# Kernel optimization log

Hardware: AMD Instinct MI355X
Metric: run time of the kernel (lower is better)

Reference implementation:

```python
import jax, jax.numpy as jnp
import numpy as np

B, S, D, H = 2, 2048, 1024, 16
HD = D // H  # head dim = 64


def setup_inputs() -> dict:
    key = jax.random.key(0)
    k1, k2, k3, k4 = jax.random.split(key, 4)
    x = jax.random.normal(k1, (B, S, D), dtype=jnp.float32)
    context = jax.random.normal(k2, (B, S, D), dtype=jnp.float32)
    Wq = jax.random.normal(k3, (D, D), dtype=jnp.float32) * 0.02   # to_query weight [out,in]
    Wkv = jax.random.normal(k4, (2 * D, D), dtype=jnp.float32) * 0.02  # to_key_value weight [out,in]
    return {"x": x, "context": context, "Wq": Wq, "Wkv": Wkv}


def reference(x, context, Wq, Wkv):
    b, i, _ = x.shape
    j = context.shape[1]
    # projections (torch Linear: y = x @ W.T)
    q = x @ Wq.T                      # [b, i, D]
    kv = context @ Wkv.T              # [b, j, 2D]
    k, v = kv[..., :D], kv[..., D:]
    # split heads: (h c) ordering -> reshape last dim to [H, HD]
    q = q.reshape(b, i, H, HD).transpose(0, 2, 1, 3)  # [b,h,i,c]
    k = k.reshape(b, j, H, HD).transpose(0, 2, 1, 3)  # [b,h,j,c]
    v = v.reshape(b, j, H, HD).transpose(0, 2, 1, 3)  # [b,h,j,c]
    q = q * (HD ** -0.5)
    scores = jnp.einsum('bhic,bhjc->bhij', q, k)      # [b,h,i,j]
    scores = scores - jax.lax.stop_gradient(scores.max(axis=-1, keepdims=True))
    attn = jax.nn.softmax(scores, axis=-1)
    out = jnp.einsum('bhij,bhjc->bhic', attn, v)      # [b,h,i,c]
    out = out.transpose(0, 2, 1, 3).reshape(b, i, H * HD)  # 'b h n d -> b n (h d)'
    return out
```

## Files before the change

### kernel.cpp

```cpp
#include <hip/hip_runtime.h>
#include <hip/hip_bf16.h>
#include <stdint.h>

typedef unsigned short u16;
typedef __attribute__((ext_vector_type(8))) __bf16 bf16x8;
typedef __attribute__((ext_vector_type(4))) float f32x4;
typedef __attribute__((ext_vector_type(16))) float f32x16;

#define AS1(p) ((const __attribute__((address_space(1))) void*)(p))
#define AS3(p) ((__attribute__((address_space(3))) void*)(p))

__device__ __forceinline__ u16 f2bf(float f) {
  union { float f; uint32_t u; } c; c.f = f;
  uint32_t u = c.u;
  u += 0x7fffu + ((u >> 16) & 1u);
  return (u16)(u >> 16);
}

__device__ __forceinline__ float exp2_fast(float x) {
  float r; asm("v_exp_f32 %0, %1" : "=v"(r) : "v"(x)); return r;
}

__global__ __launch_bounds__(256) void cast4_f32_bf16(
    const float4* __restrict__ s0, ushort4* __restrict__ d0, int n0,
    const float4* __restrict__ s1, ushort4* __restrict__ d1, int n1,
    const float4* __restrict__ s2, ushort4* __restrict__ d2, int n2,
    const float4* __restrict__ s3, ushort4* __restrict__ d3, int n3) {
  int bid = blockIdx.x;
  const float4* src; ushort4* dst; int n4, b0, nb;
  if (bid < 512)       { src = s0; dst = d0; n4 = n0; b0 = 0;    nb = 512; }
  else if (bid < 1024) { src = s1; dst = d1; n4 = n1; b0 = 512;  nb = 512; }
  else if (bid < 1152) { src = s2; dst = d2; n4 = n2; b0 = 1024; nb = 128; }
  else                 { src = s3; dst = d3; n4 = n3; b0 = 1152; nb = 256; }
  int stride = nb * 256;
  for (int i = (bid - b0) * 256 + threadIdx.x; i < n4; i += stride) {
    float4 v = src[i];
    ushort4 o;
    o.x = f2bf(v.x); o.y = f2bf(v.y); o.z = f2bf(v.z); o.w = f2bf(v.w);
    dst[i] = o;
  }
}

__global__ __launch_bounds__(256) void gemm_fused(const u16* __restrict__ xb,
                                                  const u16* __restrict__ wqb,
                                                  u16* __restrict__ qo,
                                                  const u16* __restrict__ cb,
                                                  const u16* __restrict__ wkb,
                                                  u16* __restrict__ kvo,
                                                  float scale_q) {
  __shared__ u16 As[2][128 * 32];
  __shared__ u16 Bs[2][128 * 32];
  const int K = 1024;
  int bid = blockIdx.x;
  const u16 *A, *B; u16* C; int N, bm, bn; float scale;
  if (bid < 256) { A = xb; B = wqb; C = qo;  N = 1024; bm = bid >> 3; bn = bid & 7;  scale = scale_q; }
  else { int b2 = bid - 256; A = cb; B = wkb; C = kvo; N = 2048; bm = b2 >> 4; bn = b2 & 15; scale = 1.0f; }

  int tid = threadIdx.x;
  int w = tid >> 6, l = tid & 63;
  int wr = w >> 1, wc = w & 1;
  int lr = l & 15, lg = l >> 4;

  const u16* Abase = A + (size_t)(bm * 128 + (l >> 2)) * K + (l & 3) * 8;
  const u16* Bbase = B + (size_t)(bn * 128 + (l >> 2)) * K + (l & 3) * 8;

  f32x4 acc[4][4];
#pragma unroll
  for (int i = 0; i < 4; ++i)
#pragma unroll
    for (int j = 0; j < 4; ++j) acc[i][j] = (f32x4){0.f, 0.f, 0.f, 0.f};

#define STAGE(buf, k0)                                                              \
  {                                                                                 \
    _Pragma("unroll")                                                               \
    for (int t2 = 0; t2 < 2; ++t2) {                                                \
      int seg = w * 2 + t2;                                                         \
      __builtin_amdgcn_global_load_lds(AS1(Abase + (size_t)seg * 16 * K + (k0)),    \
                                       AS3(&As[buf][seg * 512]), 16, 0, 0);         \
      __builtin_amdgcn_global_load_lds(AS1(Bbase + (size_t)seg * 16 * K + (k0)),    \
                                       AS3(&Bs[buf][seg * 512]), 16, 0, 0);         \
    }                                                                               \
  }

  STAGE(0, 0);
  for (int t = 0; t < 32; ++t) {
    int cur = t & 1;
    if (t < 31) {
      STAGE(cur ^ 1, (t + 1) * 32);
      asm volatile("s_waitcnt vmcnt(4)" ::: "memory");
    } else {
      asm volatile("s_waitcnt vmcnt(0)" ::: "memory");
    }
    __builtin_amdgcn_s_barrier();
    bf16x8 af[4], bb[4];
#pragma unroll
    for (int i = 0; i < 4; ++i)
      af[i] = *(const bf16x8*)(&As[cur][(wr * 64 + i * 16 + lr) * 32 + lg * 8]);
#pragma unroll
    for (int j = 0; j < 4; ++j)
      bb[j] = *(const bf16x8*)(&Bs[cur][(wc * 64 + j * 16 + lr) * 32 + lg * 8]);
    asm volatile("s_waitcnt lgkmcnt(0)" ::: "memory");
    __builtin_amdgcn_sched_barrier(0);
#pragma unroll
    for (int i = 0; i < 4; ++i)
#pragma unroll
      for (int j = 0; j < 4; ++j)
        acc[i][j] = __builtin_amdgcn_mfma_f32_16x16x32_bf16(af[i], bb[j], acc[i][j], 0, 0, 0);
    __builtin_amdgcn_s_barrier();
  }
#undef STAGE

#pragma unroll
  for (int i = 0; i < 4; ++i)
#pragma unroll
    for (int j = 0; j < 4; ++j)
#pragma unroll
      for (int r = 0; r < 4; ++r) {
        int row = bm * 128 + wr * 64 + i * 16 + lg * 4 + r;
        int col = bn * 128 + wc * 64 + j * 16 + lr;
        C[(size_t)row * N + col] = f2bf(acc[i][j][r] * scale);
      }
}

#define SQ 2048

__global__ __launch_bounds__(256, 2) void attn_kernel(const u16* __restrict__ Q,
                                                      const u16* __restrict__ KV,
                                                      float* __restrict__ O) {
  __shared__ u16 Ks[2 * 64 * 64];
  __shared__ u16 Vt[2 * 64 * 64];

  int qt = blockIdx.x & 15;
  int bh = blockIdx.x >> 4;
  int b = bh >> 4, h = bh & 15;
  int tid = threadIdx.x;
  int w = tid >> 6, l = tid & 63;
  int li = l & 31, hi = l >> 5;
  int jr = l >> 3, bk = l & 7;

  const u16* kbase = KV + (size_t)b * SQ * 2048 + (size_t)h * 64;
  const u16* vbase = kbase + 1024;
  int i0g = qt * 128 + w * 32;
  const u16* qrow = Q + (size_t)(b * SQ + i0g + li) * 1024 + h * 64;

  bf16x8 qf0 = *(const bf16x8*)(qrow + 0  + hi * 8);
  bf16x8 qf1 = *(const bf16x8*)(qrow + 16 + hi * 8);
  bf16x8 qf2 = *(const bf16x8*)(qrow + 32 + hi * 8);
  bf16x8 qf3 = *(const bf16x8*)(qrow + 48 + hi * 8);

  {
    const u16* gk0 = kbase + (size_t)(w * 8 + jr) * 2048 + ((bk ^ jr) * 8);
    __builtin_amdgcn_global_load_lds(AS1(gk0), AS3(Ks + w * 512), 16, 0, 0);
    const u16* gk1 = kbase + (size_t)(32 + w * 8 + jr) * 2048 + ((bk ^ jr) * 8);
    __builtin_amdgcn_global_load_lds(AS1(gk1), AS3(Ks + 2048 + w * 512), 16, 0, 0);
  }
  uint4 vregA = *(const uint4*)(vbase + (size_t)(tid >> 3) * 2048 + (tid & 7) * 8);
  uint4 vregB = *(const uint4*)(vbase + (size_t)(32 + (tid >> 3)) * 2048 + (tid & 7) * 8);

  float m_run = -1e30f, l_run = 0.f;
  f32x16 acc0, acc1;
#pragma unroll
  for (int r = 0; r < 16; ++r) { acc0[r] = 0.f; acc1[r] = 0.f; }

  for (int t = 0; t < SQ / 64; ++t) {
    int cur = t & 1;
    u16* Ksc = Ks + cur * 4096;
    u16* Vtc = Vt + cur * 4096;
    __syncthreads();
    {
      int a = tid & 7, jj0 = tid >> 3;
      const u16* pa_ = (const u16*)&vregA;
#pragma unroll
      for (int e = 0; e < 8; ++e)
        *(u16*)((char*)Vtc + (a * 8 + e) * 128 + ((jj0 * 2) ^ ((e ^ a) << 4))) = pa_[e];
      const u16* pb_ = (const u16*)&vregB;
      int jj1 = 32 + jj0;
#pragma unroll
      for (int e = 0; e < 8; ++e)
        *(u16*)((char*)Vtc + (a * 8 + e) * 128 + ((jj1 * 2) ^ ((e ^ a) << 4))) = pb_[e];
    }
    __syncthreads();
    if (t + 1 < SQ / 64) {
      int nxt = cur ^ 1;
      int j0n = (t + 1) * 64;
      const u16* gk0 = kbase + (size_t)(j0n + w * 8 + jr) * 2048 + ((bk ^ jr) * 8);
      __builtin_amdgcn_global_load_lds(AS1(gk0), AS3(Ks + nxt * 4096 + w * 512), 16, 0, 0);
      const u16* gk1 = kbase + (size_t)(j0n + 32 + w * 8 + jr) * 2048 + ((bk ^ jr) * 8);
      __builtin_amdgcn_global_load_lds(AS1(gk1), AS3(Ks + nxt * 4096 + 2048 + w * 512), 16, 0, 0);
      vregA = *(const uint4*)(vbase + (size_t)(j0n + (tid >> 3)) * 2048 + (tid & 7) * 8);
      vregB = *(const uint4*)(vbase + (size_t)(j0n + 32 + (tid >> 3)) * 2048 + (tid & 7) * 8);
    }
    f32x16 s0, s1;
#pragma unroll
    for (int r = 0; r < 16; ++r) { s0[r] = 0.f; s1[r] = 0.f; }
    int swk = (li & 7) << 4;
    __builtin_amdgcn_s_setprio(1);
#pragma unroll
    for (int kb = 0; kb < 4; ++kb) {
      bf16x8 k0 = *(const bf16x8*)((const char*)Ksc + li * 128        + ((kb * 32 + hi * 16) ^ swk));
      bf16x8 k1 = *(const bf16x8*)((const char*)Ksc + (32 + li) * 128 + ((kb * 32 + hi * 16) ^ swk));
      bf16x8 qq = (kb == 0) ? qf0 : (kb == 1) ? qf1 : (kb == 2) ? qf2 : qf3;
      s0 = __builtin_amdgcn_mfma_f32_32x32x16_bf16(k0, qq, s0, 0, 0, 0);
      s1 = __builtin_amdgcn_mfma_f32_32x32x16_bf16(k1, qq, s1, 0, 0, 0);
    }
    __builtin_amdgcn_s_setprio(0);
    float pm = fmaxf(s0[0], s0[1]);
#pragma unroll
    for (int r = 2; r < 16; r += 2) pm = fmaxf(fmaxf(pm, s0[r]), s0[r + 1]);
#pragma unroll
    for (int r = 0; r < 16; r += 2) pm = fmaxf(fmaxf(pm, s1[r]), s1[r + 1]);
    pm = fmaxf(pm, __shfl_xor(pm, 32));
    if (!__all(pm <= m_run + 8.0f)) {
      float mnew = fmaxf(m_run, pm);
      float esc = exp2_fast(m_run - mnew);
      m_run = mnew;
      l_run *= esc;
#pragma unroll
      for (int r = 0; r < 16; ++r) { acc0[r] *= esc; acc1[r] *= esc; }
    }
    float p0[16], p1[16];
    float sum = 0.f;
#pragma unroll
    for (int r = 0; r < 16; ++r) { p0[r] = exp2_fast(s0[r] - m_run); sum += p0[r]; }
#pragma unroll
    for (int r = 0; r < 16; ++r) { p1[r] = exp2_fast(s1[r] - m_run); sum += p1[r]; }
    sum += __shfl_xor(sum, 32);
    l_run += sum;
    unsigned pw[16];
#pragma unroll
    for (int i2 = 0; i2 < 8; ++i2) {
      asm("v_cvt_pk_bf16_f32 %0, %1, %2" : "=v"(pw[i2])     : "v"(p0[2 * i2]), "v"(p0[2 * i2 + 1]));
      asm("v_cvt_pk_bf16_f32 %0, %1, %2" : "=v"(pw[8 + i2]) : "v"(p1[2 * i2]), "v"(p1[2 * i2 + 1]));
    }
#pragma unroll
    for (int gB = 0; gB < 2; ++gB) {
      int o = gB * 8;
      asm volatile("v_permlane32_swap_b32 %0, %1" : "+v"(pw[o + 0]), "+v"(pw[o + 2]));
      asm volatile("v_permlane32_swap_b32 %0, %1" : "+v"(pw[o + 1]), "+v"(pw[o + 3]));
      asm volatile("v_permlane32_swap_b32 %0, %1" : "+v"(pw[o + 4]), "+v"(pw[o + 6]));
      asm volatile("v_permlane32_swap_b32 %0, %1" : "+v"(pw[o + 5]), "+v"(pw[o + 7]));
    }
    __builtin_amdgcn_s_setprio(1);
#pragma unroll
    for (int kb2 = 0; kb2 < 4; ++kb2) {
      uint4 ufr;
      ufr.x = pw[kb2 * 4 + 0]; ufr.y = pw[kb2 * 4 + 1];
      ufr.z = pw[kb2 * 4 + 2]; ufr.w = pw[kb2 * 4 + 3];
      bf16x8 pa = *(bf16x8*)&ufr;
      int jbyte = kb2 * 32 + hi * 16;
      int d0_ = li, d1_ = 32 + li;
      bf16x8 v0 = *(const bf16x8*)((const char*)Vtc + d0_ * 128 + (jbyte ^ (((d0_ ^ (d0_ >> 3)) & 7) << 4)));
      bf16x8 v1 = *(const bf16x8*)((const char*)Vtc + d1_ * 128 + (jbyte ^ (((d1_ ^ (d1_ >> 3)) & 7) << 4)));
      acc0 = __builtin_amdgcn_mfma_f32_32x32x16_bf16(v0, pa, acc0, 0, 0, 0);
      acc1 = __builtin_amdgcn_mfma_f32_32x32x16_bf16(v1, pa, acc1, 0, 0, 0);
    }
    __builtin_amdgcn_s_setprio(0);
  }
  float inv = 1.f / l_run;
  float* orow = O + ((size_t)(b * SQ + i0g + li) * 1024 + h * 64);
#pragma unroll
  for (int g = 0; g < 4; ++g) {
    f32x4 o0, o1;
#pragma unroll
    for (int q_ = 0; q_ < 4; ++q_) {
      o0[q_] = acc0[g * 4 + q_] * inv;
      o1[q_] = acc1[g * 4 + q_] * inv;
    }
    *(f32x4*)(orow + 8 * g + 4 * hi) = o0;
    *(f32x4*)(orow + 32 + 8 * g + 4 * hi) = o1;
  }
}

extern "C" void kernel_launch(void* const* d_in, const int* in_sizes, int n_in,
                              void* d_out, int out_size, void* d_ws, size_t ws_size,
                              hipStream_t stream) {
  (void)in_sizes; (void)n_in; (void)out_size; (void)ws_size;
  const float* x   = (const float*)d_in[0];
  const float* ctx = (const float*)d_in[1];
  const float* Wq  = (const float*)d_in[2];
  const float* Wkv = (const float*)d_in[3];
  float* out = (float*)d_out;
  char* ws = (char*)d_ws;

  u16* xb  = (u16*)(ws);
  u16* cb  = (u16*)(ws + (8ull  << 20));
  u16* wqb = (u16*)(ws + (16ull << 20));
  u16* wkb = (u16*)(ws + (18ull << 20));
  u16* q   = (u16*)(ws + (22ull << 20));
  u16* kv  = (u16*)(ws + (30ull << 20));

  cast4_f32_bf16<<<1408, 256, 0, stream>>>(
      (const float4*)x,   (ushort4*)xb,  (4096 * 1024) / 4,
      (const float4*)ctx, (ushort4*)cb,  (4096 * 1024) / 4,
      (const float4*)Wq,  (ushort4*)wqb, (1024 * 1024) / 4,
      (const float4*)Wkv, (ushort4*)wkb, (2048 * 1024) / 4);

  gemm_fused<<<768, 256, 0, stream>>>(xb, wqb, q, cb, wkb, kv, 0.125f * 1.44269504f);

  attn_kernel<<<512, 256, 0, stream>>>(q, kv, out);
}
```

Before: 114.1 us.

## Triple-buffer GEMM, remap blocks across XCDs, widen attention KV tile to 128

The projection GEMM moves from double to triple-buffered LDS staging with a two-tile prefetch depth, and remaps block IDs so consecutive blocks spread across the 8 XCDs. The attention kernel doubles its K/V tile from 64 to 128 keys per iteration, which halves the loop trips, barriers and softmax rescale checks. It also gives the attention kernel the same XCD-aware block remapping and restructures the QK^T MFMA chains. In exchange LDS use and register pressure rise (four score accumulators, 32 packed words), which could lower occupancy under the 2-blocks-per-CU bound.

Result: faster. 99.01 us (-13.3%).

```diff
diff --git a/kernel.cpp b/kernel.cpp
--- a/kernel.cpp
+++ b/kernel.cpp
@@ -48,10 +48,10 @@
                                                   const u16* __restrict__ wkb,
                                                   u16* __restrict__ kvo,
                                                   float scale_q) {
-  __shared__ u16 As[2][128 * 32];
-  __shared__ u16 Bs[2][128 * 32];
+  __shared__ u16 As[3][128 * 32];
+  __shared__ u16 Bs[3][128 * 32];
   const int K = 1024;
-  int bid = blockIdx.x;
+  int bid = (blockIdx.x & 7) * 96 + (blockIdx.x >> 3);
   const u16 *A, *B; u16* C; int N, bm, bn; float scale;
   if (bid < 256) { A = xb; B = wqb; C = qo;  N = 1024; bm = bid >> 3; bn = bid & 7;  scale = scale_q; }
   else { int b2 = bid - 256; A = cb; B = wkb; C = kvo; N = 2048; bm = b2 >> 4; bn = b2 & 15; scale = 1.0f; }
@@ -83,10 +83,14 @@
   }
 
   STAGE(0, 0);
+  STAGE(1, 32);
+  int cur = 0;
   for (int t = 0; t < 32; ++t) {
-    int cur = t & 1;
-    if (t < 31) {
-      STAGE(cur ^ 1, (t + 1) * 32);
+    if (t < 30) {
+      int pf = cur + 2; if (pf >= 3) pf -= 3;
+      STAGE(pf, (t + 2) * 32);
+      asm volatile("s_waitcnt vmcnt(8)" ::: "memory");
+    } else if (t == 30) {
       asm volatile("s_waitcnt vmcnt(4)" ::: "memory");
     } else {
       asm volatile("s_waitcnt vmcnt(0)" ::: "memory");
@@ -107,6 +111,7 @@
       for (int j = 0; j < 4; ++j)
         acc[i][j] = __builtin_amdgcn_mfma_f32_16x16x32_bf16(af[i], bb[j], acc[i][j], 0, 0, 0);
     __builtin_amdgcn_s_barrier();
+    if (++cur == 3) cur = 0;
   }
 #undef STAGE
 
@@ -123,20 +128,23 @@
 }
 
 #define SQ 2048
+#define NTT 16
 
 __global__ __launch_bounds__(256, 2) void attn_kernel(const u16* __restrict__ Q,
                                                       const u16* __restrict__ KV,
                                                       float* __restrict__ O) {
-  __shared__ u16 Ks[2 * 64 * 64];
-  __shared__ u16 Vt[2 * 64 * 64];
-
-  int qt = blockIdx.x & 15;
-  int bh = blockIdx.x >> 4;
+  __shared__ u16 Ks[2][128 * 64];
+  __shared__ u16 Vt[2][64 * 128];
+
+  int wgid = (blockIdx.x & 7) * 64 + (blockIdx.x >> 3);
+  int qt = wgid & 15;
+  int bh = wgid >> 4;
   int b = bh >> 4, h = bh & 15;
   int tid = threadIdx.x;
   int w = tid >> 6, l = tid & 63;
   int li = l & 31, hi = l >> 5;
   int jr = l >> 3, bk = l & 7;
+  int a7 = tid & 7, jj = tid >> 3;
 
   const u16* kbase = KV + (size_t)b * SQ * 2048 + (size_t)h * 64;
   const u16* vbase = kbase + 1024;
@@ -148,67 +156,88 @@
   bf16x8 qf2 = *(const bf16x8*)(qrow + 32 + hi * 8);
   bf16x8 qf3 = *(const bf16x8*)(qrow + 48 + hi * 8);
 
-  {
-    const u16* gk0 = kbase + (size_t)(w * 8 + jr) * 2048 + ((bk ^ jr) * 8);
-    __builtin_amdgcn_global_load_lds(AS1(gk0), AS3(Ks + w * 512), 16, 0, 0);
-    const u16* gk1 = kbase + (size_t)(32 + w * 8 + jr) * 2048 + ((bk ^ jr) * 8);
-    __builtin_amdgcn_global_load_lds(AS1(gk1), AS3(Ks + 2048 + w * 512), 16, 0, 0);
-  }
-  uint4 vregA = *(const uint4*)(vbase + (size_t)(tid >> 3) * 2048 + (tid & 7) * 8);
-  uint4 vregB = *(const uint4*)(vbase + (size_t)(32 + (tid >> 3)) * 2048 + (tid & 7) * 8);
+#pragma unroll
+  for (int c = 0; c < 4; ++c) {
+    const u16* gk = kbase + (size_t)(c * 32 + w * 8 + jr) * 2048 + ((bk ^ jr) * 8);
+    __builtin_amdgcn_global_load_lds(AS1(gk), AS3(&Ks[0][c * 2048 + w * 512]), 16, 0, 0);
+  }
+  uint4 vrA = *(const uint4*)(vbase + (size_t)(jj +  0) * 2048 + a7 * 8);
+  uint4 vrB = *(const uint4*)(vbase + (size_t)(jj + 32) * 2048 + a7 * 8);
+  uint4 vrC = *(const uint4*)(vbase + (size_t)(jj + 64) * 2048 + a7 * 8);
+  uint4 vrD = *(const uint4*)(vbase + (size_t)(jj + 96) * 2048 + a7 * 8);
 
   float m_run = -1e30f, l_run = 0.f;
-  f32x16 acc0, acc1;
-#pragma unroll
-  for (int r = 0; r < 16; ++r) { acc0[r] = 0.f; acc1[r] = 0.f; }
-
-  for (int t = 0; t < SQ / 64; ++t) {
-    int cur = t & 1;
-    u16* Ksc = Ks + cur * 4096;
-    u16* Vtc = Vt + cur * 4096;
+  f32x16 acc0, acc1, zz;
+#pragma unroll
+  for (int r = 0; r < 16; ++r) { acc0[r] = 0.f; acc1[r] = 0.f; zz[r] = 0.f; }
+
+  int swk = (li & 7) << 4;
+  int sw0 = ((li ^ (li >> 3)) & 7) << 4;
+  int sw1 = (((32 + li) ^ ((32 + li) >> 3)) & 7) << 4;
+
+  for (int t = 0; t < NTT; ++t) {
+    u16* Ksc = (u16*)Ks[t & 1];
+    char* Vtc = (char*)Vt[t & 1];
     __syncthreads();
     {
-      int a = tid & 7, jj0 = tid >> 3;
-      const u16* pa_ = (const u16*)&vregA;
-#pragma unroll
-      for (int e = 0; e < 8; ++e)
-        *(u16*)((char*)Vtc + (a * 8 + e) * 128 + ((jj0 * 2) ^ ((e ^ a) << 4))) = pa_[e];
-      const u16* pb_ = (const u16*)&vregB;
-      int jj1 = 32 + jj0;
-#pragma unroll
-      for (int e = 0; e < 8; ++e)
-        *(u16*)((char*)Vtc + (a * 8 + e) * 128 + ((jj1 * 2) ^ ((e ^ a) << 4))) = pb_[e];
-    }
-    __syncthreads();
-    if (t + 1 < SQ / 64) {
-      int nxt = cur ^ 1;
-      int j0n = (t + 1) * 64;
-      const u16* gk0 = kbase + (size_t)(j0n + w * 8 + jr) * 2048 + ((bk ^ jr) * 8);
-      __builtin_amdgcn_global_load_lds(AS1(gk0), AS3(Ks + nxt * 4096 + w * 512), 16, 0, 0);
-      const u16* gk1 = kbase + (size_t)(j0n + 32 + w * 8 + jr) * 2048 + ((bk ^ jr) * 8);
-      __builtin_amdgcn_global_load_lds(AS1(gk1), AS3(Ks + nxt * 4096 + 2048 + w * 512), 16, 0, 0);
-      vregA = *(const uint4*)(vbase + (size_t)(j0n + (tid >> 3)) * 2048 + (tid & 7) * 8);
-      vregB = *(const uint4*)(vbase + (size_t)(j0n + 32 + (tid >> 3)) * 2048 + (tid & 7) * 8);
-    }
-    f32x16 s0, s1;
-#pragma unroll
-    for (int r = 0; r < 16; ++r) { s0[r] = 0.f; s1[r] = 0.f; }
-    int swk = (li & 7) << 4;
+      const u16* pA = (const u16*)&vrA;
+      const u16* pB = (const u16*)&vrB;
+      const u16* pC = (const u16*)&vrC;
+      const u16* pD = (const u16*)&vrD;
+#pragma unroll
+      for (int e = 0; e < 8; ++e) {
+        int dbyte = (a7 * 8 + e) * 256, sw = (e ^ a7) << 4;
+        *(u16*)(Vtc + dbyte + (((jj * 2) +   0) ^ sw)) = pA[e];
+        *(u16*)(Vtc + dbyte + (((jj * 2) +  64) ^ sw)) = pB[e];
+        *(u16*)(Vtc + dbyte + (((jj * 2) + 128) ^ sw)) = pC[e];
+        *(u16*)(Vtc + dbyte + (((jj * 2) + 192) ^ sw)) = pD[e];
+      }
+    }
+    asm volatile("s_waitcnt lgkmcnt(0)" ::: "memory");
+    __builtin_amdgcn_s_barrier();
+    if (t + 1 < NTT) {
+      int j0n = (t + 1) * 128;
+      u16* Ksn = (u16*)Ks[(t + 1) & 1];
+#pragma unroll
+      for (int c = 0; c < 4; ++c) {
+        const u16* gk = kbase + (size_t)(j0n + c * 32 + w * 8 + jr) * 2048 + ((bk ^ jr) * 8);
+        __builtin_amdgcn_global_load_lds(AS1(gk), AS3(&Ksn[c * 2048 + w * 512]), 16, 0, 0);
+      }
+      vrA = *(const uint4*)(vbase + (size_t)(j0n + jj +  0) * 2048 + a7 * 8);
+      vrB = *(const uint4*)(vbase + (size_t)(j0n + jj + 32) * 2048 + a7 * 8);
+      vrC = *(const uint4*)(vbase + (size_t)(j0n + jj + 64) * 2048 + a7 * 8);
+      vrD = *(const uint4*)(vbase + (size_t)(j0n + jj + 96) * 2048 + a7 * 8);
+    }
+    f32x16 s0, s1, s2, s3;
     __builtin_amdgcn_s_setprio(1);
-#pragma unroll
-    for (int kb = 0; kb < 4; ++kb) {
-      bf16x8 k0 = *(const bf16x8*)((const char*)Ksc + li * 128        + ((kb * 32 + hi * 16) ^ swk));
-      bf16x8 k1 = *(const bf16x8*)((const char*)Ksc + (32 + li) * 128 + ((kb * 32 + hi * 16) ^ swk));
-      bf16x8 qq = (kb == 0) ? qf0 : (kb == 1) ? qf1 : (kb == 2) ? qf2 : qf3;
-      s0 = __builtin_amdgcn_mfma_f32_32x32x16_bf16(k0, qq, s0, 0, 0, 0);
-      s1 = __builtin_amdgcn_mfma_f32_32x32x16_bf16(k1, qq, s1, 0, 0, 0);
-    }
+#define QKT1(sv, JB)                                                             \
+    {                                                                            \
+      const char* kr = (const char*)Ksc + ((JB) * 32 + li) * 128;                \
+      bf16x8 kk;                                                                 \
+      kk = *(const bf16x8*)(kr + ((0  + hi * 16) ^ swk));                        \
+      sv = __builtin_amdgcn_mfma_f32_32x32x16_bf16(kk, qf0, zz, 0, 0, 0);        \
+      kk = *(const bf16x8*)(kr + ((32 + hi * 16) ^ swk));                        \
+      sv = __builtin_amdgcn_mfma_f32_32x32x16_bf16(kk, qf1, sv, 0, 0, 0);        \
+      kk = *(const bf16x8*)(kr + ((64 + hi * 16) ^ swk));                        \
+      sv = __builtin_amdgcn_mfma_f32_32x32x16_bf16(kk, qf2, sv, 0, 0, 0);        \
+      kk = *(const bf16x8*)(kr + ((96 + hi * 16) ^ swk));                        \
+      sv = __builtin_amdgcn_mfma_f32_32x32x16_bf16(kk, qf3, sv, 0, 0, 0);        \
+    }
+    QKT1(s0, 0)
+    QKT1(s1, 1)
+    QKT1(s2, 2)
+    QKT1(s3, 3)
+#undef QKT1
     __builtin_amdgcn_s_setprio(0);
-    float pm = fmaxf(s0[0], s0[1]);
-#pragma unroll
-    for (int r = 2; r < 16; r += 2) pm = fmaxf(fmaxf(pm, s0[r]), s0[r + 1]);
+    float pm = fmaxf(s0[14], s0[15]);
+#pragma unroll
+    for (int r = 0; r < 14; r += 2) pm = fmaxf(fmaxf(pm, s0[r]), s0[r + 1]);
 #pragma unroll
     for (int r = 0; r < 16; r += 2) pm = fmaxf(fmaxf(pm, s1[r]), s1[r + 1]);
+#pragma unroll
+    for (int r = 0; r < 16; r += 2) pm = fmaxf(fmaxf(pm, s2[r]), s2[r + 1]);
+#pragma unroll
+    for (int r = 0; r < 16; r += 2) pm = fmaxf(fmaxf(pm, s3[r]), s3[r + 1]);
     pm = fmaxf(pm, __shfl_xor(pm, 32));
     if (!__all(pm <= m_run + 8.0f)) {
       float mnew = fmaxf(m_run, pm);
@@ -218,22 +247,27 @@
 #pragma unroll
       for (int r = 0; r < 16; ++r) { acc0[r] *= esc; acc1[r] *= esc; }
     }
-    float p0[16], p1[16];
     float sum = 0.f;
 #pragma unroll
-    for (int r = 0; r < 16; ++r) { p0[r] = exp2_fast(s0[r] - m_run); sum += p0[r]; }
-#pragma unroll
-    for (int r = 0; r < 16; ++r) { p1[r] = exp2_fast(s1[r] - m_run); sum += p1[r]; }
+    for (int r = 0; r < 16; ++r) { s0[r] = exp2_fast(s0[r] - m_run); sum += s0[r]; }
+#pragma unroll
+    for (int r = 0; r < 16; ++r) { s1[r] = exp2_fast(s1[r] - m_run); sum += s1[r]; }
+#pragma unroll
+    for (int r = 0; r < 16; ++r) { s2[r] = exp2_fast(s2[r] - m_run); sum += s2[r]; }
+#pragma unroll
+    for (int r = 0; r < 16; ++r) { s3[r] = exp2_fast(s3[r] - m_run); sum += s3[r]; }
     sum += __shfl_xor(sum, 32);
     l_run += sum;
-    unsigned pw[16];
+    unsigned pw[32];
 #pragma unroll
     for (int i2 = 0; i2 < 8; ++i2) {
-      asm("v_cvt_pk_bf16_f32 %0, %1, %2" : "=v"(pw[i2])     : "v"(p0[2 * i2]), "v"(p0[2 * i2 + 1]));
-      asm("v_cvt_pk_bf16_f32 %0, %1, %2" : "=v"(pw[8 + i2]) : "v"(p1[2 * i2]), "v"(p1[2 * i2 + 1]));
-    }
-#pragma unroll
-    for (int gB = 0; gB < 2; ++gB) {
+      asm("v_cvt_pk_bf16_f32 %0, %1, %2" : "=v"(pw[i2])      : "v"(s0[2 * i2]), "v"(s0[2 * i2 + 1]));
+      asm("v_cvt_pk_bf16_f32 %0, %1, %2" : "=v"(pw[8 + i2])  : "v"(s1[2 * i2]), "v"(s1[2 * i2 + 1]));
+      asm("v_cvt_pk_bf16_f32 %0, %1, %2" : "=v"(pw[16 + i2]) : "v"(s2[2 * i2]), "v"(s2[2 * i2 + 1]));
+      asm("v_cvt_pk_bf16_f32 %0, %1, %2" : "=v"(pw[24 + i2]) : "v"(s3[2 * i2]), "v"(s3[2 * i2 + 1]));
+    }
+#pragma unroll
+    for (int gB = 0; gB < 4; ++gB) {
       int o = gB * 8;
       asm volatile("v_permlane32_swap_b32 %0, %1" : "+v"(pw[o + 0]), "+v"(pw[o + 2]));
       asm volatile("v_permlane32_swap_b32 %0, %1" : "+v"(pw[o + 1]), "+v"(pw[o + 3]));
@@ -242,15 +276,14 @@
     }
     __builtin_amdgcn_s_setprio(1);
 #pragma unroll
-    for (int kb2 = 0; kb2 < 4; ++kb2) {
+    for (int jsp = 0; jsp < 8; ++jsp) {
       uint4 ufr;
-      ufr.x = pw[kb2 * 4 + 0]; ufr.y = pw[kb2 * 4 + 1];
-      ufr.z = pw[kb2 * 4 + 2]; ufr.w = pw[kb2 * 4 + 3];
+      ufr.x = pw[jsp * 4 + 0]; ufr.y = pw[jsp * 4 + 1];
+      ufr.z = pw[jsp * 4 + 2]; ufr.w = pw[jsp * 4 + 3];
       bf16x8 pa = *(bf16x8*)&ufr;
-      int jbyte = kb2 * 32 + hi * 16;
-      int d0_ = li, d1_ = 32 + li;
-      bf16x8 v0 = *(const bf16x8*)((const char*)Vtc + d0_ * 128 + (jbyte ^ (((d0_ ^ (d0_ >> 3)) & 7) << 4)));
-      bf16x8 v1 = *(const bf16x8*)((const char*)Vtc + d1_ * 128 + (jbyte ^ (((d1_ ^ (d1_ >> 3)) & 7) << 4)));
+      int jbyte = jsp * 32 + hi * 16;
+      bf16x8 v0 = *(const bf16x8*)(Vtc + li * 256 + (jbyte ^ sw0));
+      bf16x8 v1 = *(const bf16x8*)(Vtc + (32 + li) * 256 + (jbyte ^ sw1));
       acc0 = __builtin_amdgcn_mfma_f32_32x32x16_bf16(v0, pa, acc0, 0, 0, 0);
       acc1 = __builtin_amdgcn_mfma_f32_32x32x16_bf16(v1, pa, acc1, 0, 0, 0);
     }
```
